# Optimization experiments

Measured on AMD Instinct MI355X. Metric: run time of the kernel, lower is better.

The kernel has to match this reference:

```python
import jax, jax.numpy as jnp
import numpy as np

N = 50000      # num nodes
E = 800000     # num edges
F_IN = 128     # CONFIG.FeatureLen()
H = 100        # conv1_hide
C = 16         # CONFIG.ClassNum()
LEAKY = 0.01


def setup_inputs() -> dict:
    key = jax.random.key(0)
    k = jax.random.split(key, 4)
    x = jax.random.normal(k[0], (N, F_IN), dtype=jnp.float32)
    edge_index = jax.random.randint(k[1], (2, E), 0, N, dtype=jnp.int32)
    W1 = jax.random.normal(k[2], (F_IN, H), dtype=jnp.float32) / np.sqrt(F_IN).astype(np.float32)
    b1 = jnp.zeros((H,), dtype=jnp.float32)
    W2 = jax.random.normal(k[3], (H, C), dtype=jnp.float32) / np.sqrt(H).astype(np.float32)
    b2 = jnp.zeros((C,), dtype=jnp.float32)
    return {"x": x, "W1": W1, "b1": b1, "W2": W2, "b2": b2, "edge_index": edge_index}


def _gcn_conv(x, W, b, src, dst):
    """PyG GCNConv: x' = D^{-1/2}(A+I)D^{-1/2} X W + b (symmetric norm, self-loops)."""
    x = x @ W  # transform first (smaller feature dim for propagation)
    loop = jnp.arange(N, dtype=src.dtype)
    s = jnp.concatenate([src, loop])  # sources (message senders)
    d = jnp.concatenate([dst, loop])  # targets (message receivers)
    deg = jax.ops.segment_sum(jnp.ones_like(d, dtype=x.dtype), d, num_segments=N)
    dinv = jnp.where(deg > 0, jax.lax.rsqrt(deg), 0.0)
    norm = dinv[s] * dinv[d]                      # [E+N]
    msg = x[s] * norm[:, None]                    # gather + scale
    out = jax.ops.segment_sum(msg, d, num_segments=N)  # scatter-add
    return out + b


def reference(x, W1, b1, W2, b2, edge_index):
    src, dst = edge_index[0], edge_index[1]
    h = _gcn_conv(x, W1, b1, src, dst)
    h = jax.nn.leaky_relu(h, negative_slope=LEAKY)
    # dropout is identity in eval mode (training=False)
    h = _gcn_conv(h, W2, b2, src, dst)
    return jax.nn.log_softmax(h, axis=1)
```

## Files before the change

### kernel.cpp

```cpp
#include <hip/hip_runtime.h>

#define F_IN 128
#define HDIM 100
#define HPAD 128
#define CDIM 16
#define CAP  96
#define BT_STRIDE 136

static constexpr float LEAKY = 0.01f;

using short8  = __attribute__((ext_vector_type(8))) short;
using float4v = __attribute__((ext_vector_type(4))) float;
using float2v = __attribute__((ext_vector_type(2))) float;

__device__ __forceinline__ unsigned short f2bf(float f) {
    unsigned u = __float_as_uint(f);
    u += 0x7fffu + ((u >> 16) & 1u);
    return (unsigned short)(u >> 16);
}


__global__ void k_fill(const int* __restrict__ src, const int* __restrict__ dst,
                       int* __restrict__ cursor, unsigned short* __restrict__ slots, int E) {
    int i = blockIdx.x * blockDim.x + threadIdx.x;
    if (i < E) {
        int d = dst[i];
        int pos = atomicAdd(&cursor[d], 1);
        slots[(size_t)d * CAP + pos] = (unsigned short)src[i];
    }
}


__global__ __launch_bounds__(256) void k_gemm1(const float* __restrict__ x,
                                               const float* __restrict__ W1,
                                               unsigned char* __restrict__ y1f8,
                                               const int* __restrict__ cursor,
                                               float* __restrict__ dinv, int N) {
    int t = threadIdx.x;
    int gid = blockIdx.x * 256 + t;
    if (gid < N) dinv[gid] = rsqrtf((float)cursor[gid] + 1.0f);

    __shared__ unsigned short Bt[F_IN * BT_STRIDE];
    for (int idx = t; idx < F_IN * HPAD; idx += 256) {
        int k = idx >> 7;
        int n = idx & 127;
        float v = (n < HDIM) ? W1[k * HDIM + n] : 0.f;
        Bt[n * BT_STRIDE + k] = f2bf(v);
    }
    __syncthreads();

    int wave = t >> 6, lane = t & 63;
    int Mtiles = (N + 15) >> 4;
    int tile = blockIdx.x * 4 + wave;
    if (tile >= Mtiles) return;
    int row0 = tile * 16;

    int m = lane & 15;
    int kq = lane >> 4;
    int arow = min(row0 + m, N - 1);
    const float* xrow = x + (size_t)arow * F_IN;

    short8 afrag[4];
    #pragma unroll
    for (int kt = 0; kt < 4; ++kt) {
        int kb = kt * 32 + kq * 8;
        float4 a0 = *(const float4*)(xrow + kb);
        float4 a1 = *(const float4*)(xrow + kb + 4);
        short8 f;
        f[0] = (short)f2bf(a0.x); f[1] = (short)f2bf(a0.y);
        f[2] = (short)f2bf(a0.z); f[3] = (short)f2bf(a0.w);
        f[4] = (short)f2bf(a1.x); f[5] = (short)f2bf(a1.y);
        f[6] = (short)f2bf(a1.z); f[7] = (short)f2bf(a1.w);
        afrag[kt] = f;
    }

    bool full = (row0 + 15 < N);
    #pragma unroll
    for (int ct = 0; ct < 8; ++ct) {
        float4v acc = {0.f, 0.f, 0.f, 0.f};
        #pragma unroll
        for (int kt = 0; kt < 4; ++kt) {
            short8 b = *(const short8*)&Bt[(ct * 16 + m) * BT_STRIDE + kt * 32 + kq * 8];
            acc = __builtin_amdgcn_mfma_f32_16x16x32_bf16(afrag[kt], b, acc, 0, 0, 0);
        }
        #pragma unroll
        for (int i = 0; i < 4; ++i) {
            int r = row0 + kq * 4 + i;
            int v8 = __builtin_amdgcn_cvt_pk_fp8_f32(acc[i], acc[i], 0, false);
            if (full || r < N)
                y1f8[(size_t)r * HPAD + ct * 16 + m] = (unsigned char)(v8 & 0xff);
        }
    }
}


__global__ __launch_bounds__(256) void k_agg1y2(const unsigned* __restrict__ y1u,
                                                const float* __restrict__ b1,
                                                const float* __restrict__ W2,
                                                const int* __restrict__ cursor,
                                                const float* __restrict__ dinv,
                                                const unsigned short* __restrict__ slots,
                                                float* __restrict__ y2, int N) {
    __shared__ float W2s[HDIM * CDIM];
    __shared__ float hs[4][2][HPAD];
    int t = threadIdx.x;
    for (int idx = t; idx < HDIM * CDIM; idx += 256) W2s[idx] = W2[idx];
    __syncthreads();

    int wave = t >> 6, lane = t & 63;
    int half = lane >> 5, l = lane & 31;
    int hbase = lane & 32;
    int n = blockIdx.x * 8 + wave * 2 + half;
    bool valid = (n < N);
    int nn = valid ? n : (N - 1);

    int beg = nn * CAP;
    int cnt = valid ? cursor[nn] : 0;
    float dn = dinv[nn];

    int cother = __shfl(cnt, lane ^ 32);
    int cmax = max(cnt, cother);

    float a0 = 0.f, a1 = 0.f, a2 = 0.f, a3 = 0.f;
    for (int e0 = 0; e0 < cmax; e0 += 32) {
        int mm = min(32, cnt - e0);
        unsigned su = 0u; float wv = 0.f;
        if (l < mm) {
            su = slots[beg + e0 + l];
            wv = dinv[su];
        }
        int mmax = min(32, cmax - e0);
        int mpad = (mmax + 7) & ~7;
        for (int j = 0; j < mpad; j += 8) {
            float w[8]; unsigned vv[8];
            #pragma unroll
            for (int q = 0; q < 8; ++q) {
                int ln = hbase | (j + q);
                unsigned s = (unsigned)__shfl((int)su, ln);
                w[q] = __shfl(wv, ln);
                vv[q] = y1u[(size_t)s * 32 + l];
            }
            #pragma unroll
            for (int q = 0; q < 8; ++q) {
                float2v lo = __builtin_amdgcn_cvt_pk_f32_fp8((int)vv[q], false);
                float2v hi = __builtin_amdgcn_cvt_pk_f32_fp8((int)vv[q], true);
                a0 = fmaf(w[q], lo[0], a0);
                a1 = fmaf(w[q], lo[1], a1);
                a2 = fmaf(w[q], hi[0], a2);
                a3 = fmaf(w[q], hi[1], a3);
            }
        }
    }
    {
        unsigned vn = y1u[(size_t)nn * 32 + l];
        float2v lo = __builtin_amdgcn_cvt_pk_f32_fp8((int)vn, false);
        float2v hi = __builtin_amdgcn_cvt_pk_f32_fp8((int)vn, true);
        a0 = fmaf(dn, lo[0], a0);
        a1 = fmaf(dn, lo[1], a1);
        a2 = fmaf(dn, hi[0], a2);
        a3 = fmaf(dn, hi[1], a3);
    }

    float4 bb = (l < 25) ? *(const float4*)&b1[4 * l] : make_float4(0.f, 0.f, 0.f, 0.f);
    float h0 = fmaf(dn, a0, bb.x);
    float h1 = fmaf(dn, a1, bb.y);
    float h2 = fmaf(dn, a2, bb.z);
    float h3 = fmaf(dn, a3, bb.w);
    h0 = h0 > 0.f ? h0 : LEAKY * h0;
    h1 = h1 > 0.f ? h1 : LEAKY * h1;
    h2 = h2 > 0.f ? h2 : LEAKY * h2;
    h3 = h3 > 0.f ? h3 : LEAKY * h3;
    *(float4*)&hs[wave][half][4 * l] = make_float4(h0, h1, h2, h3);
    __builtin_amdgcn_wave_barrier();

    int c = l & 15, kg = l >> 4;
    const float* hrow = hs[wave][half];
    float p = 0.f;
    #pragma unroll 10
    for (int j = 0; j < 50; ++j) {
        int k = 2 * j + kg;
        p = fmaf(hrow[k], W2s[k * CDIM + c], p);
    }
    p += __shfl_down(p, 16);
    if (l < 16 && valid) y2[(size_t)n * CDIM + c] = p;
}


__global__ __launch_bounds__(256) void k_agg2(const float* __restrict__ y2,
                                              const float* __restrict__ b2,
                                              const int* __restrict__ cursor,
                                              const float* __restrict__ dinv,
                                              const unsigned short* __restrict__ slots,
                                              float* __restrict__ out, int N) {
    int t = threadIdx.x;
    int wave = t >> 6, lane = t & 63;
    int sub = lane >> 4, c = lane & 15;
    int n = blockIdx.x * 16 + wave * 4 + sub;
    bool valid = (n < N);
    int nn = valid ? n : 0;

    int beg = nn * CAP;
    int cnt = valid ? cursor[nn] : 0;
    float dn = dinv[nn];
    float acc = dn * y2[(size_t)nn * CDIM + c];

    for (int e0 = 0; e0 < cnt; e0 += 16) {
        int mm = min(16, cnt - e0);
        unsigned su = 0u; float wv = 0.f;
        if (c < mm) {
            su = slots[beg + e0 + c];
            wv = dinv[su];
        }
        int mpad = (mm + 3) & ~3;
        for (int j = 0; j < mpad; j += 4) {
            float w[4]; float v[4];
            #pragma unroll
            for (int q = 0; q < 4; ++q) {
                int ln = sub * 16 + j + q;
                unsigned s = (unsigned)__shfl((int)su, ln);
                w[q] = __shfl(wv, ln);
                v[q] = y2[(size_t)s * CDIM + c];
            }
            #pragma unroll
            for (int q = 0; q < 4; ++q) acc = fmaf(w[q], v[q], acc);
        }
    }

    float lg = fmaf(dn, acc, b2[c]);
    float mx = lg;
    #pragma unroll
    for (int k = 8; k; k >>= 1) mx = fmaxf(mx, __shfl_xor(mx, k));
    float ex = __expf(lg - mx);
    #pragma unroll
    for (int k = 8; k; k >>= 1) ex += __shfl_xor(ex, k);
    float lse = mx + __logf(ex);
    if (valid) out[(size_t)n * CDIM + c] = lg - lse;
}


extern "C" void kernel_launch(void* const* d_in, const int* in_sizes, int n_in,
                              void* d_out, int out_size, void* d_ws, size_t ws_size,
                              hipStream_t stream) {
    const float* x  = (const float*)d_in[0];
    const float* W1 = (const float*)d_in[1];
    const float* b1 = (const float*)d_in[2];
    const float* W2 = (const float*)d_in[3];
    const float* b2 = (const float*)d_in[4];
    const int*   ei = (const int*)d_in[5];

    const int N = in_sizes[0] / F_IN;
    const int E = in_sizes[5] / 2;
    const int* src = ei;
    const int* dst = ei + E;

    char* ws = (char*)d_ws;
    size_t off = 0;
    auto alloc = [&](size_t bytes) {
        char* p = ws + off;
        off += (bytes + 255) & ~(size_t)255;
        return p;
    };
    int*            cursor = (int*)alloc((size_t)N * 4);
    float*          dinv   = (float*)alloc((size_t)N * 4);
    unsigned char*  y1f8   = (unsigned char*)alloc((size_t)N * HPAD);
    float*          y2     = (float*)alloc((size_t)N * CDIM * 4);
    unsigned short* slots  = (unsigned short*)alloc((size_t)N * CAP * 2);
    (void)ws_size; (void)n_in; (void)out_size;

    int Mtiles = (N + 15) / 16;

    hipMemsetAsync(cursor, 0, (size_t)N * 4, stream);
    k_fill<<<(E + 255) / 256, 256, 0, stream>>>(src, dst, cursor, slots, E);
    k_gemm1<<<(Mtiles + 3) / 4, 256, 0, stream>>>(x, W1, y1f8, cursor, dinv, N);
    k_agg1y2<<<(N + 7) / 8, 256, 0, stream>>>((const unsigned*)y1f8, b1, W2,
                                              cursor, dinv, slots, y2, N);
    k_agg2<<<(N + 15) / 16, 256, 0, stream>>>(y2, b2, cursor, dinv, slots,
                                              (float*)d_out, N);
}
```

Before: 189.2 us.

## Fuse edge fill into GEMM1 launch with XCD-partitioned destination ranges

Merges the CSR slot-fill kernel and the first GEMM into one launch. Extra blocks do the fill, and each block handles one of 8 destination-node ranges chosen by blockIdx&7, which looks aimed at keeping a range's atomics within one XCD's L2. The separate dinv array is dropped; consumers recompute rsqrt(deg+1) from the degree counts on the fly. In exchange, every fill block rescans its whole edge chunk, so the dst array is read eight times, and the aggregation loops gain extra rsqrt work.

```diff
diff --git a/kernel.cpp b/kernel.cpp
--- a/kernel.cpp
+++ b/kernel.cpp
@@ -6,6 +6,7 @@
 #define CDIM 16
 #define CAP  96
 #define BT_STRIDE 136
+#define GF 2048
 
 static constexpr float LEAKY = 0.01f;
 
@@ -20,27 +21,36 @@
 }
 
 
-__global__ void k_fill(const int* __restrict__ src, const int* __restrict__ dst,
-                       int* __restrict__ cursor, unsigned short* __restrict__ slots, int E) {
-    int i = blockIdx.x * blockDim.x + threadIdx.x;
-    if (i < E) {
-        int d = dst[i];
-        int pos = atomicAdd(&cursor[d], 1);
-        slots[(size_t)d * CAP + pos] = (unsigned short)src[i];
-    }
-}
-
-
-__global__ __launch_bounds__(256) void k_gemm1(const float* __restrict__ x,
-                                               const float* __restrict__ W1,
-                                               unsigned char* __restrict__ y1f8,
-                                               const int* __restrict__ cursor,
-                                               float* __restrict__ dinv, int N) {
+__global__ __launch_bounds__(256) void k_fill_gemm1(const float* __restrict__ x,
+                                                    const float* __restrict__ W1,
+                                                    unsigned char* __restrict__ y1f8,
+                                                    const int* __restrict__ src,
+                                                    const int* __restrict__ dst,
+                                                    int* __restrict__ cursor,
+                                                    unsigned short* __restrict__ slots,
+                                                    int N, int E, int GG) {
+    __shared__ unsigned short Bt[F_IN * BT_STRIDE];
+    int bx = blockIdx.x;
     int t = threadIdx.x;
-    int gid = blockIdx.x * 256 + t;
-    if (gid < N) dinv[gid] = rsqrtf((float)cursor[gid] + 1.0f);
-
-    __shared__ unsigned short Bt[F_IN * BT_STRIDE];
+
+    if (bx >= GG) {
+        int fb    = bx - GG;
+        int part  = bx & 7;
+        int chunk = fb >> 3;
+        int nper  = (N + 7) >> 3;
+        int lo = part * nper, hi = min(N, lo + nper);
+        int ecb = (E + (GF >> 3) - 1) >> 8;
+        int e0 = chunk * ecb, e1 = min(E, e0 + ecb);
+        for (int i = e0 + t; i < e1; i += 256) {
+            int d = dst[i];
+            if (d >= lo && d < hi) {
+                int pos = atomicAdd(&cursor[d], 1);
+                slots[(size_t)d * CAP + pos] = (unsigned short)src[i];
+            }
+        }
+        return;
+    }
+
     for (int idx = t; idx < F_IN * HPAD; idx += 256) {
         int k = idx >> 7;
         int n = idx & 127;
@@ -51,7 +61,7 @@
 
     int wave = t >> 6, lane = t & 63;
     int Mtiles = (N + 15) >> 4;
-    int tile = blockIdx.x * 4 + wave;
+    int tile = bx * 4 + wave;
     if (tile >= Mtiles) return;
     int row0 = tile * 16;
 
@@ -97,8 +107,7 @@
 __global__ __launch_bounds__(256) void k_agg1y2(const unsigned* __restrict__ y1u,
                                                 const float* __restrict__ b1,
                                                 const float* __restrict__ W2,
-                                                const int* __restrict__ cursor,
-                                                const float* __restrict__ dinv,
+                                                const int* __restrict__ deg,
                                                 const unsigned short* __restrict__ slots,
                                                 float* __restrict__ y2, int N) {
     __shared__ float W2s[HDIM * CDIM];
@@ -115,8 +124,8 @@
     int nn = valid ? n : (N - 1);
 
     int beg = nn * CAP;
-    int cnt = valid ? cursor[nn] : 0;
-    float dn = dinv[nn];
+    int cnt = valid ? deg[nn] : 0;
+    float dn = rsqrtf((float)deg[nn] + 1.0f);
 
     int cother = __shfl(cnt, lane ^ 32);
     int cmax = max(cnt, cother);
@@ -127,7 +136,7 @@
         unsigned su = 0u; float wv = 0.f;
         if (l < mm) {
             su = slots[beg + e0 + l];
-            wv = dinv[su];
+            wv = rsqrtf((float)deg[su] + 1.0f);
         }
         int mmax = min(32, cmax - e0);
         int mpad = (mmax + 7) & ~7;
@@ -142,23 +151,23 @@
             }
             #pragma unroll
             for (int q = 0; q < 8; ++q) {
-                float2v lo = __builtin_amdgcn_cvt_pk_f32_fp8((int)vv[q], false);
-                float2v hi = __builtin_amdgcn_cvt_pk_f32_fp8((int)vv[q], true);
-                a0 = fmaf(w[q], lo[0], a0);
-                a1 = fmaf(w[q], lo[1], a1);
-                a2 = fmaf(w[q], hi[0], a2);
-                a3 = fmaf(w[q], hi[1], a3);
+                float2v lov = __builtin_amdgcn_cvt_pk_f32_fp8((int)vv[q], false);
+                float2v hiv = __builtin_amdgcn_cvt_pk_f32_fp8((int)vv[q], true);
+                a0 = fmaf(w[q], lov[0], a0);
+                a1 = fmaf(w[q], lov[1], a1);
+                a2 = fmaf(w[q], hiv[0], a2);
+                a3 = fmaf(w[q], hiv[1], a3);
             }
         }
     }
     {
         unsigned vn = y1u[(size_t)nn * 32 + l];
-        float2v lo = __builtin_amdgcn_cvt_pk_f32_fp8((int)vn, false);
-        float2v hi = __builtin_amdgcn_cvt_pk_f32_fp8((int)vn, true);
-        a0 = fmaf(dn, lo[0], a0);
-        a1 = fmaf(dn, lo[1], a1);
-        a2 = fmaf(dn, hi[0], a2);
-        a3 = fmaf(dn, hi[1], a3);
+        float2v lov = __builtin_amdgcn_cvt_pk_f32_fp8((int)vn, false);
+        float2v hiv = __builtin_amdgcn_cvt_pk_f32_fp8((int)vn, true);
+        a0 = fmaf(dn, lov[0], a0);
+        a1 = fmaf(dn, lov[1], a1);
+        a2 = fmaf(dn, hiv[0], a2);
+        a3 = fmaf(dn, hiv[1], a3);
     }
 
     float4 bb = (l < 25) ? *(const float4*)&b1[4 * l] : make_float4(0.f, 0.f, 0.f, 0.f);
@@ -188,8 +197,7 @@
 
 __global__ __launch_bounds__(256) void k_agg2(const float* __restrict__ y2,
                                               const float* __restrict__ b2,
-                                              const int* __restrict__ cursor,
-                                              const float* __restrict__ dinv,
+                                              const int* __restrict__ deg,
                                               const unsigned short* __restrict__ slots,
                                               float* __restrict__ out, int N) {
     int t = threadIdx.x;
@@ -200,8 +208,8 @@
     int nn = valid ? n : 0;
 
     int beg = nn * CAP;
-    int cnt = valid ? cursor[nn] : 0;
-    float dn = dinv[nn];
+    int cnt = valid ? deg[nn] : 0;
+    float dn = rsqrtf((float)deg[nn] + 1.0f);
     float acc = dn * y2[(size_t)nn * CDIM + c];
 
     for (int e0 = 0; e0 < cnt; e0 += 16) {
@@ -209,7 +217,7 @@
         unsigned su = 0u; float wv = 0.f;
         if (c < mm) {
             su = slots[beg + e0 + c];
-            wv = dinv[su];
+            wv = rsqrtf((float)deg[su] + 1.0f);
         }
         int mpad = (mm + 3) & ~3;
         for (int j = 0; j < mpad; j += 4) {
@@ -261,19 +269,18 @@
         return p;
     };
     int*            cursor = (int*)alloc((size_t)N * 4);
-    float*          dinv   = (float*)alloc((size_t)N * 4);
     unsigned char*  y1f8   = (unsigned char*)alloc((size_t)N * HPAD);
     float*          y2     = (float*)alloc((size_t)N * CDIM * 4);
     unsigned short* slots  = (unsigned short*)alloc((size_t)N * CAP * 2);
     (void)ws_size; (void)n_in; (void)out_size;
 
     int Mtiles = (N + 15) / 16;
+    int GG = (Mtiles + 3) / 4;
 
     hipMemsetAsync(cursor, 0, (size_t)N * 4, stream);
-    k_fill<<<(E + 255) / 256, 256, 0, stream>>>(src, dst, cursor, slots, E);
-    k_gemm1<<<(Mtiles + 3) / 4, 256, 0, stream>>>(x, W1, y1f8, cursor, dinv, N);
+    k_fill_gemm1<<<GG + GF, 256, 0, stream>>>(x, W1, y1f8, src, dst, cursor, slots, N, E, GG);
     k_agg1y2<<<(N + 7) / 8, 256, 0, stream>>>((const unsigned*)y1f8, b1, W2,
-                                              cursor, dinv, slots, y2, N);
-    k_agg2<<<(N + 15) / 16, 256, 0, stream>>>(y2, b2, cursor, dinv, slots,
+                                              cursor, slots, y2, N);
+    k_agg2<<<(N + 15) / 16, 256, 0, stream>>>(y2, b2, cursor, slots,
                                               (float*)d_out, N);
 }
```

Measured after the change: 175.7 us. 7.1% less time.
